# Optimization experiments

Hardware: AMD Instinct MI355X
Metric: run time of the kernel (lower is better)

Reference implementation:

```python
import jax, jax.numpy as jnp
import numpy as np

N_HEAD = 16
D_HEAD = 64
D_LATENT = 32
BLOCK_SIZE = 2048


def rope_cache(dim, max_seq_len, theta=10000.0):
    inv_freq = 1.0 / (theta ** (jnp.arange(0, dim, 2, dtype=jnp.float32) / dim))
    t = jnp.arange(max_seq_len, dtype=jnp.float32)
    freqs = jnp.einsum('i,j->ij', t, inv_freq)        # [T, dim/2]
    emb = jnp.concatenate([freqs, freqs], axis=-1)    # [T, dim]
    return jnp.cos(emb), jnp.sin(emb)


def apply_rope(x, cos, sin):
    # x: [B, H, T, C]; interleaved-pair rotation as in the torch module
    B, H, T, C = x.shape
    c = cos[:T][None, None]
    s = sin[:T][None, None]
    x1 = x[..., 0::2]
    x2 = x[..., 1::2]
    rotated = jnp.stack((-x2, x1), axis=-1).reshape(B, H, T, C)
    return x * c + rotated * s


def setup_inputs() -> dict:
    key = jax.random.key(0)
    ks = jax.random.split(key, 7)
    sd = 0.02
    return {
        'x':   jax.random.normal(ks[0], (2, 2048, 1024), dtype=jnp.float32),
        'Wq':  jax.random.normal(ks[1], (1024, 1024), dtype=jnp.float32) * sd,
        'Wk':  jax.random.normal(ks[2], (512, 1024), dtype=jnp.float32) * sd,
        'Wv':  jax.random.normal(ks[3], (512, 1024), dtype=jnp.float32) * sd,
        'Wku': jax.random.normal(ks[4], (64, 32), dtype=jnp.float32) * sd,
        'Wvu': jax.random.normal(ks[5], (64, 32), dtype=jnp.float32) * sd,
        'Wc':  jax.random.normal(ks[6], (1024, 1024), dtype=jnp.float32) * sd,
    }


def reference(x, Wq, Wk, Wv, Wku, Wvu, Wc):
    B, T, C = x.shape
    H, Dh, Dl = N_HEAD, D_HEAD, D_LATENT

    # latent KV (compressed cache entries)
    k_lat = (x @ Wk.T).reshape(B, T, H, Dl)   # [B,T,H,Dl]
    v_lat = (x @ Wv.T).reshape(B, T, H, Dl)

    # q and up-projected k/v -> [B,H,T,Dh]
    q = (x @ Wq.T).reshape(B, T, H, Dh).transpose(0, 2, 1, 3)
    k = jnp.einsum('bthl,dl->bhtd', k_lat, Wku)
    v = jnp.einsum('bthl,dl->bhtd', v_lat, Wvu)

    cos, sin = rope_cache(Dh, BLOCK_SIZE)
    q = apply_rope(q, cos, sin)
    k = apply_rope(k, cos, sin)

    scale = 1.0 / jnp.sqrt(jnp.asarray(Dh, dtype=x.dtype))
    att = jnp.einsum('bhqd,bhkd->bhqk', q, k) * scale   # [B,H,T,T]
    causal = jnp.tril(jnp.ones((T, T), dtype=bool))
    att = jnp.where(causal[None, None], att, -jnp.inf)
    att = jax.nn.softmax(att, axis=-1)

    y = jnp.einsum('bhqk,bhkd->bhqd', att, v)           # [B,H,T,Dh]
    y = y.transpose(0, 2, 1, 3).reshape(B, T, C) @ Wc.T  # [B,T,C]
    return y, k_lat, v_lat
```

## Files before the change

### kernel.cpp

```cpp
#include <hip/hip_runtime.h>
#include <math.h>

#define NHEAD  16
#define DHEAD  64
#define DLAT   32
#define TSEQ   2048
#define NBATCH 2
#define CDIM   1024
#define MROWS  (NBATCH*TSEQ)

typedef __attribute__((ext_vector_type(8))) short bf16x8;
typedef __attribute__((ext_vector_type(4))) short bf16x4;
typedef __attribute__((ext_vector_type(4))) float f32x4;

#define AS1 __attribute__((address_space(1)))
#define AS3 __attribute__((address_space(3)))

__device__ __forceinline__ unsigned short f2bf(float f) {
    union { float f; unsigned u; } v; v.f = f;
    unsigned r = v.u + 0x7fff + ((v.u >> 16) & 1);
    return (unsigned short)(r >> 16);
}

__device__ __forceinline__ unsigned pk2(float lo, float hi) {
    return (unsigned)f2bf(lo) | ((unsigned)f2bf(hi) << 16);
}

__device__ __forceinline__ unsigned pack_trunc(float hi, float lo) {
    return __builtin_amdgcn_perm(__float_as_uint(hi), __float_as_uint(lo), 0x07060302u);
}

__device__ __forceinline__ void gld_lds16(const unsigned short* g, unsigned short* l) {
    __builtin_amdgcn_global_load_lds((const AS1 void*)g, (AS3 void*)l, 16, 0, 0);
}

__device__ __forceinline__ f32x4 mfma_16x16x16_bf16(bf16x4 a, bf16x4 b, f32x4 c) {
#if __has_builtin(__builtin_amdgcn_mfma_f32_16x16x16bf16_1k)
    return __builtin_amdgcn_mfma_f32_16x16x16bf16_1k(a, b, c, 0, 0, 0);
#else
    asm volatile("v_mfma_f32_16x16x16_bf16 %0, %1, %2, %0\n\ts_nop 4"
                 : "+v"(c) : "v"(a), "v"(b));
    return c;
#endif
}

#define QSCALE 0.18033688011112042f
#define RFREQ  0.28782313662425572f

__global__ __launch_bounds__(256) void cvt_all(
        const float* __restrict__ x,  const float* __restrict__ wq,
        const float* __restrict__ wk, const float* __restrict__ wv,
        const float* __restrict__ wc, const float* __restrict__ wku,
        const float* __restrict__ wvu,
        unsigned short* __restrict__ xb, unsigned short* __restrict__ wall) {
    int i = (blockIdx.x * 256 + threadIdx.x) * 4;
    const float* src; unsigned short* dst; int off;
    if      (i < 4194304) { src = x;   dst = xb;             off = 0;       }
    else if (i < 5242880) { src = wq;  dst = wall;           off = 4194304; }
    else if (i < 5767168) { src = wk;  dst = wall + 1048576; off = 5242880; }
    else if (i < 6291456) { src = wv;  dst = wall + 1572864; off = 5767168; }
    else if (i < 7340032) { src = wc;  dst = wall + 2097152; off = 6291456; }
    else if (i < 7342080) { src = wku; dst = wall + 3145728; off = 7340032; }
    else                  { src = wvu; dst = wall + 3147776; off = 7342080; }
    float4 v = *(const float4*)(src + (i - off));
    ushort4 o = { f2bf(v.x), f2bf(v.y), f2bf(v.z), f2bf(v.w) };
    *(ushort4*)(dst + (i - off)) = o;
}

__device__ __forceinline__ void gemm_core_128(
        const unsigned short* __restrict__ A, const unsigned short* __restrict__ W,
        int K, int bm, int bn, unsigned short* As, unsigned short* Bs,
        f32x4 (&acc)[4][2]) {
    const int tid = threadIdx.x;
    const int w = tid >> 6, lane = tid & 63;
    const int quad = lane >> 4, l16 = lane & 15;
    const int wm = (w >> 2) * 64, wn = (w & 3) * 32;

    const int r8 = lane >> 3, c8 = lane & 7;
    const int scl = (c8 ^ r8) * 8;

    const unsigned short* Ag0 = A + (size_t)(bm +      w*8 + r8) * K + scl;
    const unsigned short* Ag1 = A + (size_t)(bm + 64 + w*8 + r8) * K + scl;
    const unsigned short* Wg0 = W + (size_t)(bn +      w*8 + r8) * K + scl;
    const unsigned short* Wg1 = W + (size_t)(bn + 64 + w*8 + r8) * K + scl;
    unsigned short* AsD0 = &As[(     w*8) * 64];
    unsigned short* AsD1 = &As[(64 + w*8) * 64];
    unsigned short* BsD0 = &Bs[(     w*8) * 64];
    unsigned short* BsD1 = &Bs[(64 + w*8) * 64];

    const int fx0 = (quad ^ (l16 & 7)) * 8;
    const int fx1 = ((quad + 4) ^ (l16 & 7)) * 8;

    const int nt = K >> 6;

    gld_lds16(Ag0, AsD0);
    gld_lds16(Ag1, AsD1);
    gld_lds16(Wg0, BsD0);
    gld_lds16(Wg1, BsD1);
    __syncthreads();

    for (int t = 0; t < nt; ++t) {
        const int buf = t & 1;
        if (t + 1 < nt) {
            const int k0 = (t + 1) * 64;
            gld_lds16(Ag0 + k0, AsD0 + (buf^1)*8192);
            gld_lds16(Ag1 + k0, AsD1 + (buf^1)*8192);
            gld_lds16(Wg0 + k0, BsD0 + (buf^1)*8192);
            gld_lds16(Wg1 + k0, BsD1 + (buf^1)*8192);
        }
        const unsigned short* Ab = As + buf*8192;
        const unsigned short* Bb = Bs + buf*8192;
        bf16x8 af0[4], af1[4], bf0[2], bf1[2];
        #pragma unroll
        for (int t2 = 0; t2 < 4; ++t2) {
            af0[t2] = *(const bf16x8*)&Ab[(wm + t2*16 + l16)*64 + fx0];
            af1[t2] = *(const bf16x8*)&Ab[(wm + t2*16 + l16)*64 + fx1];
        }
        #pragma unroll
        for (int c = 0; c < 2; ++c) {
            bf0[c] = *(const bf16x8*)&Bb[(wn + c*16 + l16)*64 + fx0];
            bf1[c] = *(const bf16x8*)&Bb[(wn + c*16 + l16)*64 + fx1];
        }
        #pragma unroll
        for (int t2 = 0; t2 < 4; ++t2)
            #pragma unroll
            for (int c = 0; c < 2; ++c) {
                acc[t2][c] = __builtin_amdgcn_mfma_f32_16x16x32_bf16(af0[t2], bf0[c], acc[t2][c], 0, 0, 0);
                acc[t2][c] = __builtin_amdgcn_mfma_f32_16x16x32_bf16(af1[t2], bf1[c], acc[t2][c], 0, 0, 0);
            }
        __syncthreads();
    }
}

__device__ __forceinline__ void gemm_core(
        const unsigned short* __restrict__ A, const unsigned short* __restrict__ W,
        int K, int bm, int bn, unsigned short* As, unsigned short* Bs,
        f32x4 (&acc)[2][2]) {
    const int tid = threadIdx.x;
    const int w = tid >> 6, lane = tid & 63;
    const int quad = lane >> 4, l16 = lane & 15;
    const int wm = (w >> 1) * 32, wn = (w & 1) * 32;

    const int r8 = lane >> 3, c8 = lane & 7;
    const int scl = (c8 ^ r8) * 8;

    const unsigned short* Ag0 = A + (size_t)(bm +      w*8 + r8) * K + scl;
    const unsigned short* Ag1 = A + (size_t)(bm + 64 + w*8 + r8) * K + scl;
    const unsigned short* Wg0 = W + (size_t)(bn +      w*8 + r8) * K + scl;
    unsigned short* AsD0 = &As[(     w*8) * 64];
    unsigned short* AsD1 = &As[(64 + w*8) * 64];
    unsigned short* BsD  = &Bs[(     w*8) * 64];

    const int fx0 = (quad ^ (l16 & 7)) * 8;
    const int fx1 = ((quad + 4) ^ (l16 & 7)) * 8;

    const int nt = K >> 6;

    gld_lds16(Ag0, AsD0);
    gld_lds16(Ag1, AsD1);
    gld_lds16(Wg0, BsD);
    __syncthreads();

    for (int t = 0; t < nt; ++t) {
        const int buf = t & 1;
        if (t + 1 < nt) {
            const int k0 = (t + 1) * 64;
            gld_lds16(Ag0 + k0, AsD0 + (buf^1)*8192);
            gld_lds16(Ag1 + k0, AsD1 + (buf^1)*8192);
            gld_lds16(Wg0 + k0, BsD  + (buf^1)*4096);
        }
        const unsigned short* Ab = As + buf*8192;
        const unsigned short* Bb = Bs + buf*4096;
        bf16x8 af0[2], af1[2], bf0[2], bf1[2];
        #pragma unroll
        for (int t2 = 0; t2 < 2; ++t2) {
            af0[t2] = *(const bf16x8*)&Ab[(wm + t2*16 + l16)*64 + fx0];
            af1[t2] = *(const bf16x8*)&Ab[(wm + t2*16 + l16)*64 + fx1];
        }
        #pragma unroll
        for (int c = 0; c < 2; ++c) {
            bf0[c] = *(const bf16x8*)&Bb[(wn + c*16 + l16)*64 + fx0];
            bf1[c] = *(const bf16x8*)&Bb[(wn + c*16 + l16)*64 + fx1];
        }
        #pragma unroll
        for (int t2 = 0; t2 < 2; ++t2)
            #pragma unroll
            for (int c = 0; c < 2; ++c) {
                acc[t2][c] = __builtin_amdgcn_mfma_f32_16x16x32_bf16(af0[t2], bf0[c], acc[t2][c], 0, 0, 0);
                acc[t2][c] = __builtin_amdgcn_mfma_f32_16x16x32_bf16(af1[t2], bf1[c], acc[t2][c], 0, 0, 0);
            }
        __syncthreads();
    }
}

__global__ __launch_bounds__(512, 4) void gemm_proj(
        const unsigned short* __restrict__ A, const unsigned short* __restrict__ W,
        unsigned short* __restrict__ qbo, float* __restrict__ okl,
        float* __restrict__ ovl, int K) {
    __shared__ unsigned short As[2*128*64];
    __shared__ unsigned short Bs[2*128*64];
    const int bm = blockIdx.y * 128, bn = blockIdx.x * 128;
    f32x4 acc[4][2] = {};
    gemm_core_128(A, W, K, bm, bn, As, Bs, acc);

    const int tid = threadIdx.x;
    const int w = tid >> 6, lane = tid & 63;
    const int quad = lane >> 4, l16 = lane & 15;
    const int wm = (w >> 2) * 64, wn = (w & 3) * 32;

    if (bn < 1024) {
        const int p = l16 & 1;
        const float invf0 = __expf(-(float)(l16)      * RFREQ);
        const float invf1 = __expf(-(float)(16 + l16) * RFREQ);
        #pragma unroll
        for (int t = 0; t < 4; ++t)
            #pragma unroll
            for (int r = 0; r < 4; ++r) {
                int row = bm + wm + t*16 + quad*4 + r;
                int ts  = row & 2047;
                float tf = (float)ts;
                #pragma unroll
                for (int c = 0; c < 2; ++c) {
                    int col = bn + wn + c*16 + l16;
                    int h   = col >> 6;
                    int d   = col & 63;
                    float x  = acc[t][c][r];
                    float px = __shfl_xor(x, 1, 64);
                    float sv, cv;
                    __sincosf(tf * (c ? invf1 : invf0), &sv, &cv);
                    float o = (x*cv + (p ? px : -px)*sv) * QSCALE;
                    float po = __shfl_xor(o, 1, 64);
                    if (!p) {
                        size_t obase = (((size_t)((row >> 11)*16 + h))*TSEQ + ts)*DHEAD;
                        unsigned pr = pk2(o, po);
                        *(unsigned*)&qbo[obase + d] = pr;
                    }
                }
            }
    } else {
        #pragma unroll
        for (int t = 0; t < 4; ++t)
            #pragma unroll
            for (int c = 0; c < 2; ++c)
                #pragma unroll
                for (int r = 0; r < 4; ++r) {
                    int row = bm + wm + t*16 + quad*4 + r;
                    int col = bn + wn + c*16 + l16 - 1024;
                    float* base = (col < 512) ? okl : ovl;
                    int cc = col & 511;
                    base[(size_t)row * 512 + cc] = acc[t][c][r];
                }
    }
}

__global__ __launch_bounds__(512, 6) void gemm_out(
        const unsigned short* __restrict__ A, const unsigned short* __restrict__ W,
        float* __restrict__ O, int N, int K) {
    __shared__ unsigned short As[2*128*64];
    __shared__ unsigned short Bs[2*64*64];
    const int bm = blockIdx.y * 128, bn = blockIdx.x * 64;
    f32x4 acc[2][2] = {};
    gemm_core(A, W, K, bm, bn, As, Bs, acc);

    const int tid = threadIdx.x;
    const int w = tid >> 6, lane = tid & 63;
    const int quad = lane >> 4, l16 = lane & 15;
    const int wm = (w >> 1) * 32, wn = (w & 1) * 32;
    #pragma unroll
    for (int t = 0; t < 2; ++t)
        #pragma unroll
        for (int c = 0; c < 2; ++c)
            #pragma unroll
            for (int r = 0; r < 4; ++r) {
                int row = bm + wm + t*16 + quad*4 + r;
                int col = bn + wn + c*16 + l16;
                O[(size_t)row * N + col] = acc[t][c][r];
            }
}

__global__ __launch_bounds__(256) void latup(
        const float* __restrict__ klat, const float* __restrict__ vlat,
        const unsigned short* __restrict__ wkub, const unsigned short* __restrict__ wvub,
        unsigned short* __restrict__ kb, unsigned short* __restrict__ vt) {
    __shared__ __attribute__((aligned(16))) unsigned short ksh[4][16][72];
    __shared__ __attribute__((aligned(16))) unsigned short vsh[4][64][24];

    const int bh = blockIdx.y, b = bh >> 4, h = bh & 15;
    const int tid = threadIdx.x, w = tid >> 6, lane = tid & 63;
    const int quad = lane >> 4, l16 = lane & 15;
    const int tw = blockIdx.x * 64 + w * 16;
    const int t  = tw + l16;

    const float* klp = klat + ((size_t)(b*TSEQ + t))*(NHEAD*DLAT) + h*DLAT + quad*8;
    const float* vlp = vlat + ((size_t)(b*TSEQ + t))*(NHEAD*DLAT) + h*DLAT + quad*8;
    float4 kA = *(const float4*)klp, kB = *(const float4*)(klp + 4);
    float4 vA = *(const float4*)vlp, vB = *(const float4*)(vlp + 4);

    bf16x8 xk[4], xv[4];
    #pragma unroll
    for (int c = 0; c < 4; ++c) {
        xk[c] = *(const bf16x8*)&wkub[(c*16 + l16)*DLAT + quad*8];
        xv[c] = *(const bf16x8*)&wvub[(c*16 + l16)*DLAT + quad*8];
    }

    union { bf16x8 v; unsigned u[4]; } yk, yv;
    yk.u[0] = pk2(kA.x, kA.y); yk.u[1] = pk2(kA.z, kA.w);
    yk.u[2] = pk2(kB.x, kB.y); yk.u[3] = pk2(kB.z, kB.w);
    yv.u[0] = pk2(vA.x, vA.y); yv.u[1] = pk2(vA.z, vA.w);
    yv.u[2] = pk2(vB.x, vB.y); yv.u[3] = pk2(vB.z, vB.w);

    f32x4 aK[4], aV[4];
    #pragma unroll
    for (int c = 0; c < 4; ++c) {
        f32x4 z = {0.f, 0.f, 0.f, 0.f};
        aK[c] = __builtin_amdgcn_mfma_f32_16x16x32_bf16(xk[c], yk.v, z, 0, 0, 0);
        aV[c] = __builtin_amdgcn_mfma_f32_16x16x32_bf16(xv[c], yv.v, z, 0, 0, 0);
    }

    float C0[4], S0[4], C1[4], S1[4];
    const float tf = (float)t;
    #pragma unroll
    for (int j = 0; j < 4; ++j) {
        float f0 = (float)(quad*4 + j);
        __sincosf(tf * __expf(-f0 * RFREQ),          &S0[j], &C0[j]);
        __sincosf(tf * __expf(-(f0 + 16.f) * RFREQ), &S1[j], &C1[j]);
    }

    #pragma unroll
    for (int c = 0; c < 4; ++c) {
        const float* Cs = (c & 1) ? C1 : C0;
        const float* Ss = (c & 1) ? S1 : S0;
        float a0 = aK[c][0], a1 = aK[c][1], a2 = aK[c][2], a3 = aK[c][3];
        unsigned kw0 = pk2(a0*Cs[0] - a1*Ss[0], a1*Cs[1] + a0*Ss[1]);
        unsigned kw1 = pk2(a2*Cs[2] - a3*Ss[2], a3*Cs[3] + a2*Ss[3]);
        *(uint2*)&ksh[w][l16][c*16 + quad*4] = make_uint2(kw0, kw1);

        vsh[w][c*16 + quad*4 + 0][l16] = f2bf(aV[c][0]);
        vsh[w][c*16 + quad*4 + 1][l16] = f2bf(aV[c][1]);
        vsh[w][c*16 + quad*4 + 2][l16] = f2bf(aV[c][2]);
        vsh[w][c*16 + quad*4 + 3][l16] = f2bf(aV[c][3]);
    }

    __asm__ __volatile__("s_waitcnt lgkmcnt(0)" ::: "memory");

    const int ro = lane >> 2, co = (lane & 3) * 16;
    size_t go = ((size_t)bh*TSEQ + tw + ro)*DHEAD + co;
    int4 k0o = *(const int4*)&ksh[w][ro][co];
    int4 k1o = *(const int4*)&ksh[w][ro][co + 8];
    *(int4*)&kb[go]     = k0o;
    *(int4*)&kb[go + 8] = k1o;

    size_t vo = ((size_t)bh*DHEAD + lane)*TSEQ + tw;
    int4 v0o = *(const int4*)&vsh[w][lane][0];
    int4 v1o = *(const int4*)&vsh[w][lane][8];
    *(int4*)&vt[vo]     = v0o;
    *(int4*)&vt[vo + 8] = v1o;
}

__device__ __forceinline__ void online_sm(f32x4 (&s)[8], float& m_run, float& l_run,
                                          f32x4 (&o)[4]) {
    float mx = -1e30f;
    #pragma unroll
    for (int c = 0; c < 8; ++c)
        #pragma unroll
        for (int r = 0; r < 4; ++r) mx = fmaxf(mx, s[c][r]);
    mx = fmaxf(mx, __shfl_xor(mx, 16, 64));
    mx = fmaxf(mx, __shfl_xor(mx, 32, 64));
    if (!__all(mx <= m_run + 8.f)) {
        float mn = fmaxf(m_run, mx);
        float alpha = __builtin_exp2f(m_run - mn);
        m_run = mn;
        l_run *= alpha;
        #pragma unroll
        for (int c = 0; c < 4; ++c)
            #pragma unroll
            for (int r = 0; r < 4; ++r) o[c][r] *= alpha;
    }
    float ls = 0.f;
    #pragma unroll
    for (int c = 0; c < 8; ++c)
        #pragma unroll
        for (int r = 0; r < 4; ++r) {
            float p = __builtin_exp2f(s[c][r] - m_run);
            s[c][r] = p;
            ls += p;
        }
    ls += __shfl_xor(ls, 16, 64);
    ls += __shfl_xor(ls, 32, 64);
    l_run += ls;
}

__global__ __launch_bounds__(512, 4) void flash_attn(
        const unsigned short* __restrict__ qb, const unsigned short* __restrict__ kb,
        const unsigned short* __restrict__ vtb, unsigned short* __restrict__ yatt) {
    const int bh = blockIdx.x;
    const int b = bh >> 4, h = bh & 15;

    __shared__ unsigned short Ks[2][128][64];
    __shared__ unsigned short VTs[2][64][128];

    const int tid  = threadIdx.x;
    const int w    = tid >> 6;
    const int lane = tid & 63;
    const int quad = lane >> 4;
    const int l16  = lane & 15;
    const bool heavy = (w >= 4);
    const int wq = w & 3;

    const int qtA = blockIdx.y;
    const int qtB = 31 - qtA;
    const int qt  = heavy ? qtB : qtA;
    const int myN = (qt + 2) >> 1;
    const int nB  = (qtB + 2) >> 1;

    const unsigned short* Kbase = kb  + (size_t)bh * TSEQ * DHEAD;
    const unsigned short* Vbase = vtb + (size_t)bh * DHEAD * TSEQ;

    const int kr8 = lane >> 3, kc8 = lane & 7;
    const int kcl = (kc8 ^ kr8) * 8;
    const int vr4 = lane >> 4, vcp = lane & 15;

    const int kx0 = (quad ^ (l16 & 7)) * 8;
    const int kx1 = ((quad + 4) ^ (l16 & 7)) * 8;
    const int vq = (quad >> 1), vodd = (quad & 1) * 4;

    const unsigned short* qbase =
        qb + ((size_t)bh*TSEQ + qt*64 + wq*16 + l16) * DHEAD + quad*8;
    bf16x8 q0 = *(const bf16x8*)qbase;
    bf16x8 q1 = *(const bf16x8*)(qbase + 32);

    f32x4 oacc[4] = {};
    float m_run = -1e30f, l_run = 0.f;

    #pragma unroll
    for (int i = 0; i < 2; ++i) {
        gld_lds16(Kbase + (size_t)(w*16 + i*8 + kr8)*DHEAD + kcl,
                  &Ks[0][w*16 + i*8][0]);
        int vrow = w*8 + i*4 + vr4;
        int vcl = (vcp ^ (vrow & 15)) * 8;
        gld_lds16(Vbase + (size_t)vrow*TSEQ + vcl, &VTs[0][w*8 + i*4][0]);
    }
    __syncthreads();

    for (int j = 0; j < nB; ++j) {
        const int buf = j & 1;
        if (j + 1 < nB) {
            const int kc = (j + 1) * 128;
            #pragma unroll
            for (int i = 0; i < 2; ++i) {
                gld_lds16(Kbase + (size_t)(kc + w*16 + i*8 + kr8)*DHEAD + kcl,
                          &Ks[buf^1][w*16 + i*8][0]);
                int vrow = w*8 + i*4 + vr4;
                int vcl = (vcp ^ (vrow & 15)) * 8;
                gld_lds16(Vbase + (size_t)vrow*TSEQ + kc + vcl,
                          &VTs[buf^1][w*8 + i*4][0]);
            }
        }

        if (j < myN) {
            f32x4 s[8];
            __builtin_amdgcn_s_setprio(1);
            #pragma unroll
            for (int c = 0; c < 8; ++c) {
                bf16x8 ak0 = *(const bf16x8*)&Ks[buf][c*16 + l16][kx0];
                bf16x8 ak1 = *(const bf16x8*)&Ks[buf][c*16 + l16][kx1];
                f32x4 z = {0.f, 0.f, 0.f, 0.f};
                z = __builtin_amdgcn_mfma_f32_16x16x32_bf16(ak0, q0, z, 0, 0, 0);
                z = __builtin_amdgcn_mfma_f32_16x16x32_bf16(ak1, q1, z, 0, 0, 0);
                s[c] = z;
            }
            __builtin_amdgcn_s_setprio(0);

            if (j == myN - 1) {
                #pragma unroll
                for (int c = 0; c < 8; ++c)
                    #pragma unroll
                    for (int r = 0; r < 4; ++r)
                        if (j*128 + c*16 + quad*4 + r > qt*64 + wq*16 + l16)
                            s[c][r] = -1e30f;
            }

            online_sm(s, m_run, l_run, oacc);

            __builtin_amdgcn_s_setprio(1);
            #pragma unroll
            for (int c = 0; c < 8; ++c) {
                union { bf16x4 v; unsigned u[2]; } bP;
                bP.u[0] = pack_trunc(s[c][1], s[c][0]);
                bP.u[1] = pack_trunc(s[c][3], s[c][2]);
                const int vcol = ((2*c + vq) ^ l16) * 8 + vodd;
                #pragma unroll
                for (int dc = 0; dc < 4; ++dc) {
                    bf16x4 av = *(const bf16x4*)&VTs[buf][dc*16 + l16][vcol];
                    oacc[dc] = mfma_16x16x16_bf16(av, bP.v, oacc[dc]);
                }
            }
            __builtin_amdgcn_s_setprio(0);
        }

        __syncthreads();
    }

    float invl = 1.0f / l_run;
    unsigned short* Wt = &Ks[0][0][0] + w * (16*72);
    #pragma unroll
    for (int c = 0; c < 4; ++c)
        #pragma unroll
        for (int r = 0; r < 4; ++r)
            Wt[(size_t)l16*72 + c*16 + quad*4 + r] = f2bf(oacc[c][r] * invl);
    __asm__ __volatile__("" ::: "memory");
    #pragma unroll
    for (int p = 0; p < 2; ++p) {
        int row = p*8 + (lane >> 3);
        int d0 = (lane & 7) * 8;
        int4 val = *(const int4*)&Wt[row*72 + d0];
        int tg = qt*64 + wq*16 + row;
        *(int4*)&yatt[((size_t)(b*TSEQ + tg))*CDIM + h*DHEAD + d0] = val;
    }
}

extern "C" void kernel_launch(void* const* d_in, const int* in_sizes, int n_in,
                              void* d_out, int out_size, void* d_ws, size_t ws_size,
                              hipStream_t stream) {
    const float* x   = (const float*)d_in[0];
    const float* Wq  = (const float*)d_in[1];
    const float* Wk  = (const float*)d_in[2];
    const float* Wv  = (const float*)d_in[3];
    const float* Wku = (const float*)d_in[4];
    const float* Wvu = (const float*)d_in[5];
    const float* Wc  = (const float*)d_in[6];

    float* out_y  = (float*)d_out;
    float* out_kl = out_y  + (size_t)MROWS * CDIM;
    float* out_vl = out_kl + (size_t)MROWS * NHEAD*DLAT;

    float* qproj = (float*)d_ws;
    unsigned short* xb   = (unsigned short*)(qproj + (size_t)MROWS*CDIM);
    unsigned short* qb   = xb  + (size_t)MROWS*CDIM;
    unsigned short* kb   = qb  + (size_t)MROWS*CDIM;
    unsigned short* vt   = kb  + (size_t)MROWS*CDIM;
    unsigned short* wall = vt  + (size_t)MROWS*CDIM;
    unsigned short* wcb  = wall + (size_t)2048*CDIM;
    unsigned short* wkub = wall + 3145728;
    unsigned short* wvub = wall + 3147776;
    unsigned short* yatt = (unsigned short*)qproj;

    cvt_all<<<7172, 256, 0, stream>>>(x, Wq, Wk, Wv, Wc, Wku, Wvu, xb, wall);

    gemm_proj<<<dim3(2048/128, MROWS/128), 512, 0, stream>>>(
        xb, wall, qb, out_kl, out_vl, CDIM);

    latup<<<dim3(TSEQ/64, NBATCH*NHEAD), 256, 0, stream>>>(
        out_kl, out_vl, wkub, wvub, kb, vt);

    flash_attn<<<dim3(NBATCH*NHEAD, 16), 512, 0, stream>>>(qb, kb, vt, yatt);

    gemm_out<<<dim3(CDIM/64, MROWS/128), 512, 0, stream>>>(yatt, wcb, out_y, CDIM, CDIM);
}
```

Measured before the change: 182.6 us.

## Single-buffer flash attention K/V tiles to halve LDS and raise occupancy

Replaces the double-buffered K and V^T shared-memory tiles with a single buffer and loads each tile synchronously at the top of every iteration. The launch bound is raised from 4 to 8 blocks per CU so that more workgroups can be resident to hide load latency. This gives up the in-block prefetch overlap and may increase register pressure under the tighter launch bound.

```diff
diff --git a/kernel.cpp b/kernel.cpp
--- a/kernel.cpp
+++ b/kernel.cpp
@@ -390,14 +390,15 @@
     l_run += ls;
 }
 
-__global__ __launch_bounds__(512, 4) void flash_attn(
+__global__ __launch_bounds__(512, 8) void flash_attn(
         const unsigned short* __restrict__ qb, const unsigned short* __restrict__ kb,
         const unsigned short* __restrict__ vtb, unsigned short* __restrict__ yatt) {
     const int bh = blockIdx.x;
     const int b = bh >> 4, h = bh & 15;
 
-    __shared__ unsigned short Ks[2][128][64];
-    __shared__ unsigned short VTs[2][64][128];
+    __shared__ unsigned short SH[128*64 + 64*128];
+    unsigned short* Ks  = SH;
+    unsigned short* VTs = SH + 128*64;
 
     const int tid  = threadIdx.x;
     const int w    = tid >> 6;
@@ -432,38 +433,26 @@
     f32x4 oacc[4] = {};
     float m_run = -1e30f, l_run = 0.f;
 
-    #pragma unroll
-    for (int i = 0; i < 2; ++i) {
-        gld_lds16(Kbase + (size_t)(w*16 + i*8 + kr8)*DHEAD + kcl,
-                  &Ks[0][w*16 + i*8][0]);
-        int vrow = w*8 + i*4 + vr4;
-        int vcl = (vcp ^ (vrow & 15)) * 8;
-        gld_lds16(Vbase + (size_t)vrow*TSEQ + vcl, &VTs[0][w*8 + i*4][0]);
-    }
-    __syncthreads();
-
     for (int j = 0; j < nB; ++j) {
-        const int buf = j & 1;
-        if (j + 1 < nB) {
-            const int kc = (j + 1) * 128;
-            #pragma unroll
-            for (int i = 0; i < 2; ++i) {
-                gld_lds16(Kbase + (size_t)(kc + w*16 + i*8 + kr8)*DHEAD + kcl,
-                          &Ks[buf^1][w*16 + i*8][0]);
-                int vrow = w*8 + i*4 + vr4;
-                int vcl = (vcp ^ (vrow & 15)) * 8;
-                gld_lds16(Vbase + (size_t)vrow*TSEQ + kc + vcl,
-                          &VTs[buf^1][w*8 + i*4][0]);
-            }
-        }
+        const int kc = j * 128;
+        #pragma unroll
+        for (int i = 0; i < 2; ++i) {
+            gld_lds16(Kbase + (size_t)(kc + w*16 + i*8 + kr8)*DHEAD + kcl,
+                      &Ks[(w*16 + i*8) * 64]);
+            int vrow = w*8 + i*4 + vr4;
+            int vcl = (vcp ^ (vrow & 15)) * 8;
+            gld_lds16(Vbase + (size_t)vrow*TSEQ + kc + vcl,
+                      &VTs[(w*8 + i*4) * 128]);
+        }
+        __syncthreads();
 
         if (j < myN) {
             f32x4 s[8];
             __builtin_amdgcn_s_setprio(1);
             #pragma unroll
             for (int c = 0; c < 8; ++c) {
-                bf16x8 ak0 = *(const bf16x8*)&Ks[buf][c*16 + l16][kx0];
-                bf16x8 ak1 = *(const bf16x8*)&Ks[buf][c*16 + l16][kx1];
+                bf16x8 ak0 = *(const bf16x8*)&Ks[(c*16 + l16)*64 + kx0];
+                bf16x8 ak1 = *(const bf16x8*)&Ks[(c*16 + l16)*64 + kx1];
                 f32x4 z = {0.f, 0.f, 0.f, 0.f};
                 z = __builtin_amdgcn_mfma_f32_16x16x32_bf16(ak0, q0, z, 0, 0, 0);
                 z = __builtin_amdgcn_mfma_f32_16x16x32_bf16(ak1, q1, z, 0, 0, 0);
@@ -491,7 +480,7 @@
                 const int vcol = ((2*c + vq) ^ l16) * 8 + vodd;
                 #pragma unroll
                 for (int dc = 0; dc < 4; ++dc) {
-                    bf16x4 av = *(const bf16x4*)&VTs[buf][dc*16 + l16][vcol];
+                    bf16x4 av = *(const bf16x4*)&VTs[(dc*16 + l16)*128 + vcol];
                     oacc[dc] = mfma_16x16x16_bf16(av, bP.v, oacc[dc]);
                 }
             }
@@ -502,7 +491,7 @@
     }
 
     float invl = 1.0f / l_run;
-    unsigned short* Wt = &Ks[0][0][0] + w * (16*72);
+    unsigned short* Wt = SH + w * (16*72);
     #pragma unroll
     for (int c = 0; c < 4; ++c)
         #pragma unroll
```

New measurement: 251.4 us. +37.6%, slower.
